# Kernel tuning notes

Measured on AMD Instinct MI355X. Metric: run time of the kernel, lower is better.

## Reference

```python
import jax, jax.numpy as jnp
import numpy as np

B, S, INP, HID = 64, 2048, 512, 512

def setup_inputs() -> dict:
    key = jax.random.key(0)
    ks = jax.random.split(key, 8)
    inp = jax.random.normal(ks[0], (B, INP), dtype=jnp.float32)
    context = jax.random.normal(ks[1], (B, S, INP), dtype=jnp.float32)
    mask = jax.random.randint(ks[2], (B, S), 0, 2) == 1  # True = masked out
    lim_l = 1.0 / np.sqrt(INP)
    Wl = jax.random.uniform(ks[3], (HID, INP), minval=-lim_l, maxval=lim_l, dtype=jnp.float32)
    bl = jax.random.uniform(ks[4], (HID,), minval=-lim_l, maxval=lim_l, dtype=jnp.float32)
    Wc = jax.random.uniform(ks[5], (HID, INP), minval=-lim_l, maxval=lim_l, dtype=jnp.float32)  # Conv1d k=1 weight squeezed
    bc = jax.random.uniform(ks[6], (HID,), minval=-lim_l, maxval=lim_l, dtype=jnp.float32)
    V = jax.random.uniform(ks[7], (HID,), minval=-1.0, maxval=1.0, dtype=jnp.float32)
    return {"inp": inp, "context": context, "mask": mask,
            "Wl": Wl, "bl": bl, "Wc": Wc, "bc": bc, "V": V}

def reference(inp, context, mask, Wl, bl, Wc, bc, V):
    # hid: [B, HID], broadcast over S
    hid = inp @ Wl.T + bl
    # 1x1 Conv1d over permuted context == per-position linear: [B, HID, S]
    ctx = jnp.einsum('bsi,hi->bhs', context, Wc) + bc[None, :, None]
    # additive attention scores: [B, S]
    att = jnp.einsum('h,bhs->bs', V, jnp.tanh(hid[:, :, None] + ctx))
    att = jnp.where(mask, -jnp.inf, att)
    alpha = jax.nn.softmax(att, axis=1)
    # context vector: [B, HID]
    hidden_state = jnp.einsum('bhs,bs->bh', ctx, alpha)
    return (hidden_state, alpha)
```

## Files before the change

kernel.cpp:

```cpp
#include <hip/hip_runtime.h>
#include <hip/hip_bf16.h>
#include <cstdint>
#include <cstddef>

#define B_   64
#define S_   2048
#define INP_ 512
#define HID_ 512
#define NCH_ 32

typedef float          floatx4  __attribute__((ext_vector_type(4)));
typedef __bf16         bf16x8   __attribute__((ext_vector_type(8)));
typedef unsigned short ushortx8 __attribute__((ext_vector_type(8)));
typedef unsigned short ushortx4 __attribute__((ext_vector_type(4)));

#define K2E 1.4426950408889634f

__device__ __forceinline__ unsigned short f2bf(float f) {
  unsigned u = __float_as_uint(f);
  u += 0x7FFFu + ((u >> 16) & 1u);
  return (unsigned short)(u >> 16);
}
__device__ __forceinline__ float bf2f(unsigned short h) {
  return __uint_as_float(((unsigned)h) << 16);
}
__device__ __forceinline__ float fast_tanh(float x) {
  float u = __builtin_amdgcn_exp2f(x * 2.88539008177792681472f);
  return 1.0f - 2.0f * __builtin_amdgcn_rcpf(u + 1.0f);
}

__device__ __forceinline__ int detect_mask_mode(const void* mask, int t, int* flags) {
  if (t == 0) *flags = 0;
  __syncthreads();
  int f = 0;
  const unsigned* mw = (const unsigned*)mask;
  for (int i = t; i < 512; i += 256) {
    unsigned v = mw[i];
    if (v > 1u) f |= 1;
    if (v != 0u && v != 0x3f800000u) f |= 2;
  }
  if (f) atomicOr(flags, f);
  __syncthreads();
  const int fl = *flags;
  return ((fl & 1) == 0) ? 0 : (((fl & 2) == 0) ? 1 : 2);
}
__device__ __forceinline__ bool mask_at(const void* mask, int mode, size_t idx) {
  if (mode == 0) return ((const int*)mask)[idx] != 0;
  if (mode == 1) return ((const float*)mask)[idx] != 0.0f;
  return ((const unsigned char*)mask)[idx] != 0;
}

__global__ __launch_bounds__(256) void prep_kernel(
    const float* __restrict__ inp, const float* __restrict__ Wl,
    const float* __restrict__ bl, float* __restrict__ hid,
    const float* __restrict__ Wc, unsigned short* __restrict__ pk)
{
  __shared__ float vs[512];
  const int t = threadIdx.x;
  if (blockIdx.x < 128) {
    int g = blockIdx.x * 256 + t;
    int l = g & 63, ks = (g >> 6) & 15, m16 = g >> 10;
    int row = m16 * 16 + (l & 15);
    int kb  = ks * 32 + (l >> 4) * 8;
    const float4* s = (const float4*)(Wc + (size_t)row * 512 + kb);
    float4 a = s[0], c = s[1];
    ushortx8 o = { f2bf(a.x), f2bf(a.y), f2bf(a.z), f2bf(a.w),
                   f2bf(c.x), f2bf(c.y), f2bf(c.z), f2bf(c.w) };
    *(ushortx8*)(pk + (size_t)g * 8) = o;
    return;
  }
  const int bx = blockIdx.x - 128;
  const int xo = bx & 7, b = bx >> 3;
  const int w = t >> 6, lane = t & 63;
  for (int i = t; i < 512; i += 256) vs[i] = inp[(size_t)b * 512 + i];
  __syncthreads();
  float vl[8];
  #pragma unroll
  for (int j = 0; j < 8; ++j) vl[j] = vs[lane * 8 + j];
  const int h0 = xo * 64 + w * 16;
  #pragma unroll
  for (int i = 0; i < 16; ++i) {
    const int h = h0 + i;
    const float4* wr = (const float4*)(Wl + (size_t)h * 512 + lane * 8);
    float4 w0 = wr[0], w1 = wr[1];
    float d = w0.x*vl[0] + w0.y*vl[1] + w0.z*vl[2] + w0.w*vl[3]
            + w1.x*vl[4] + w1.y*vl[5] + w1.z*vl[6] + w1.w*vl[7];
    #pragma unroll
    for (int off = 32; off; off >>= 1) d += __shfl_xor(d, off);
    if (lane == 0) hid[(size_t)b * 512 + h] = bl[h] + d;
  }
}

__global__ __launch_bounds__(256, 2) void att_gemm_kernel(
    const float* __restrict__ context, const unsigned short* __restrict__ Wc_pk,
    const float* __restrict__ hid, const float* __restrict__ bc,
    const float* __restrict__ V, const void* __restrict__ mask,
    float* __restrict__ att, float* __restrict__ partial,
    float* __restrict__ mt, float* __restrict__ lt)
{
  __shared__ alignas(16) unsigned short bsm[64 * 512];
  __shared__ float hid_sm[512];
  __shared__ float V_sm[512];
  __shared__ float bc_sm[512];
  __shared__ float att_sm[64];
  __shared__ float w_sm[64];
  __shared__ int   flags;

  const int b    = blockIdx.y;
  const int c    = blockIdx.x;
  const int s0   = c * 64;
  const int t    = threadIdx.x;
  const int lane = t & 63;
  const int w    = t >> 6;
  const int quad = lane >> 4;
  const int l15  = lane & 15;

  const int mode = detect_mask_mode(mask, t, &flags);

  for (int i = t; i < 512; i += 256) {
    hid_sm[i] = hid[b * 512 + i];
    V_sm[i]   = V[i];
    bc_sm[i]  = bc[i];
  }
  if (t < 64) att_sm[t] = 0.0f;

  floatx4 acc[8][4];
  #pragma unroll
  for (int m = 0; m < 8; ++m)
    #pragma unroll
    for (int n = 0; n < 4; ++n) { floatx4 z = {0.f,0.f,0.f,0.f}; acc[m][n] = z; }

  const unsigned short* apBase = Wc_pk + (size_t)(w * 8) * 8192 + lane * 8;
  const float* src = context + ((size_t)b * S_ + s0) * INP_;

  for (int phase = 0; phase < 4; ++phase) {
    __syncthreads();
    #pragma unroll
    for (int i = 0; i < 8; ++i) {
      int id  = t + i * 256;
      int row = id >> 5;
      int c4  = id & 31;
      float4 f = *(const float4*)(src + (size_t)row * INP_ + phase * 128 + c4 * 4);
      int chunk = c4 >> 1, half = c4 & 1;
      int sw = chunk ^ (row & 7);
      ushortx4 hv = { f2bf(f.x), f2bf(f.y), f2bf(f.z), f2bf(f.w) };
      *(ushortx4*)(&bsm[row * 512 + phase * 128 + sw * 8 + half * 4]) = hv;
    }
    __syncthreads();
    #pragma unroll
    for (int ksl = 0; ksl < 4; ++ksl) {
      const int ksg = phase * 4 + ksl;
      bf16x8 af[8];
      #pragma unroll
      for (int m = 0; m < 8; ++m)
        af[m] = *(const bf16x8*)(apBase + (size_t)m * 8192 + ksg * 512);
      bf16x8 bfr[4];
      #pragma unroll
      for (int n = 0; n < 4; ++n) {
        int row = n * 16 + l15;
        int cc  = ksl * 4 + quad;
        bfr[n] = *(const bf16x8*)(&bsm[row * 512 + phase * 128 + ((cc ^ (row & 7)) * 8)]);
      }
      #pragma unroll
      for (int m = 0; m < 8; ++m)
        #pragma unroll
        for (int n = 0; n < 4; ++n)
          acc[m][n] = __builtin_amdgcn_mfma_f32_16x16x32_bf16(af[m], bfr[n], acc[m][n], 0, 0, 0);
    }
  }

  float attacc[4] = {0.f, 0.f, 0.f, 0.f};
  #pragma unroll
  for (int m = 0; m < 8; ++m) {
    const int hb = w * 128 + m * 16 + quad * 4;
    #pragma unroll
    for (int r = 0; r < 4; ++r) {
      const int h = hb + r;
      const float base = hid_sm[h] + bc_sm[h];
      const float vv = V_sm[h];
      #pragma unroll
      for (int n = 0; n < 4; ++n)
        attacc[n] += vv * fast_tanh(base + acc[m][n][r]);
    }
  }
  #pragma unroll
  for (int n = 0; n < 4; ++n) {
    float v = attacc[n];
    v += __shfl_xor(v, 16);
    v += __shfl_xor(v, 32);
    if (lane < 16) atomicAdd(&att_sm[n * 16 + l15], v);
  }
  __syncthreads();

  if (t < 64) {
    att[(size_t)b * S_ + s0 + t] = att_sm[t];
    const bool m = mask_at(mask, mode, (size_t)b * S_ + s0 + t);
    const float av = att_sm[t];
    float mv = m ? -1e30f : av;
    #pragma unroll
    for (int off = 32; off; off >>= 1) mv = fmaxf(mv, __shfl_xor(mv, off));
    const float wv = m ? 0.0f : __builtin_amdgcn_exp2f((av - mv) * K2E);
    w_sm[t] = wv;
    float lv = wv;
    #pragma unroll
    for (int off = 32; off; off >>= 1) lv += __shfl_xor(lv, off);
    if (t == 0) { mt[b * NCH_ + c] = mv; lt[b * NCH_ + c] = lv; }
  }
  __syncthreads();

  {
    const int k0 = t * 2;
    const int p  = k0 >> 7, kl = k0 & 127;
    const int c4 = kl >> 2, j = kl & 3;
    const int idxu = p * 128 + (c4 >> 1) * 8 + (c4 & 1) * 4 + j;
    float ax = 0.f, ay = 0.f;
    #pragma unroll 8
    for (int s = 0; s < 64; ++s) {
      const unsigned v = *(const unsigned*)(&bsm[s * 512 + (idxu ^ ((s & 7) << 3))]);
      const float wv = w_sm[s];
      ax = fmaf(wv, bf2f((unsigned short)(v & 0xffffu)), ax);
      ay = fmaf(wv, bf2f((unsigned short)(v >> 16)), ay);
    }
    float2 o; o.x = ax; o.y = ay;
    *(float2*)(partial + ((size_t)c * B_ + b) * INP_ + k0) = o;
  }
}

__global__ __launch_bounds__(256) void finalize_kernel(
    const void* __restrict__ mask, const float* __restrict__ att,
    const float* __restrict__ mt, const float* __restrict__ lt,
    float* __restrict__ sc, float* __restrict__ alpha)
{
  __shared__ int flags;
  __shared__ float Msh, Lsh;
  const int b = blockIdx.x, t = threadIdx.x;
  const int mode = detect_mask_mode(mask, t, &flags);

  if (t < 32) {
    float m = mt[b * NCH_ + t];
    #pragma unroll
    for (int off = 16; off; off >>= 1) m = fmaxf(m, __shfl_xor(m, off));
    float e = __builtin_amdgcn_exp2f((mt[b * NCH_ + t] - m) * K2E) * lt[b * NCH_ + t];
    #pragma unroll
    for (int off = 16; off; off >>= 1) e += __shfl_xor(e, off);
    if (t == 0) { Msh = m; Lsh = e; }
  }
  __syncthreads();
  const float M = Msh;
  const float rL = 1.0f / Lsh;
  if (t < 32) sc[b * NCH_ + t] = __builtin_amdgcn_exp2f((mt[b * NCH_ + t] - M) * K2E) * rL;

  #pragma unroll
  for (int i = 0; i < 8; ++i) {
    const int idx = i * 256 + t;
    const bool m = mask_at(mask, mode, (size_t)b * S_ + idx);
    const float a = m ? 0.0f
                      : __builtin_amdgcn_exp2f((att[(size_t)b * S_ + idx] - M) * K2E) * rL;
    alpha[(size_t)b * S_ + idx] = a;
  }
}

__global__ __launch_bounds__(256) void hiddendot_kernel(
    const float* __restrict__ Wc, const float* __restrict__ bc,
    const float* __restrict__ partial, const float* __restrict__ sc,
    float* __restrict__ hidden)
{
  __shared__ float vs[512];
  __shared__ float scs[NCH_];
  const int b = blockIdx.y, t = threadIdx.x;
  const int w = t >> 6, lane = t & 63;
  if (t < NCH_) scs[t] = sc[b * NCH_ + t];
  __syncthreads();
  for (int i = t; i < 512; i += 256) {
    float s = 0.0f;
    #pragma unroll 4
    for (int c = 0; c < NCH_; ++c)
      s += scs[c] * partial[((size_t)c * B_ + b) * INP_ + i];
    vs[i] = s;
  }
  __syncthreads();
  float vl[8];
  #pragma unroll
  for (int j = 0; j < 8; ++j) vl[j] = vs[lane * 8 + j];
  const int h0 = blockIdx.x * 64 + w * 16;
  #pragma unroll
  for (int i = 0; i < 16; ++i) {
    const int h = h0 + i;
    const float4* wr = (const float4*)(Wc + (size_t)h * 512 + lane * 8);
    float4 w0 = wr[0], w1 = wr[1];
    float d = w0.x*vl[0] + w0.y*vl[1] + w0.z*vl[2] + w0.w*vl[3]
            + w1.x*vl[4] + w1.y*vl[5] + w1.z*vl[6] + w1.w*vl[7];
    #pragma unroll
    for (int off = 32; off; off >>= 1) d += __shfl_xor(d, off);
    if (lane == 0) hidden[(size_t)b * 512 + h] = bc[h] + d;
  }
}

extern "C" void kernel_launch(void* const* d_in, const int* in_sizes, int n_in,
                              void* d_out, int out_size, void* d_ws, size_t ws_size,
                              hipStream_t stream)
{
  const float* inp     = (const float*)d_in[0];
  const float* context = (const float*)d_in[1];
  const void*  mask    = d_in[2];
  const float* Wl      = (const float*)d_in[3];
  const float* bl      = (const float*)d_in[4];
  const float* Wc      = (const float*)d_in[5];
  const float* bc      = (const float*)d_in[6];
  const float* V       = (const float*)d_in[7];

  float* hidden = (float*)d_out;
  float* alpha  = (float*)d_out + B_ * HID_;

  char* ws = (char*)d_ws;
  const size_t HIDW = (size_t)B_ * HID_ * 4;
  const size_t ATT  = (size_t)B_ * S_ * 4;
  const size_t PK   = (size_t)HID_ * INP_ * 2;
  const size_t PART = (size_t)NCH_ * B_ * INP_ * 4;
  const size_t MT   = (size_t)B_ * NCH_ * 4;

  float* hid_ws      = (float*)ws;
  float* att_ws      = (float*)(ws + HIDW);
  unsigned short* pk = (unsigned short*)(ws + HIDW + ATT);
  float* partial     = (float*)(ws + HIDW + ATT + PK);
  float* mt          = (float*)(ws + HIDW + ATT + PK + PART);
  float* lt          = (float*)(ws + HIDW + ATT + PK + PART + MT);
  float* sc          = (float*)(ws + HIDW + ATT + PK + PART + 2 * MT);

  prep_kernel<<<640, 256, 0, stream>>>(inp, Wl, bl, hid_ws, Wc, pk);
  att_gemm_kernel<<<dim3(NCH_, B_), 256, 0, stream>>>(
      context, pk, hid_ws, bc, V, mask, att_ws, partial, mt, lt);
  finalize_kernel<<<B_, 256, 0, stream>>>(mask, att_ws, mt, lt, sc, alpha);
  hiddendot_kernel<<<dim3(HID_ / 64, B_), 256, 0, stream>>>(Wc, bc, partial, sc, hidden);
}
```

Measured before the change: 490.8 us.

## Halve sequence tile to 32 and software-pipeline context staging into shared memory

Shrinks each attention block's sequence tile from 64 to 32 positions, which doubles the chunk count, cuts LDS and accumulator use, and raises the occupancy hint to 3 blocks per SM. The context tile is now fully kept in LDS, with the next K-phase's global loads issued before the current phase's MFMAs and written after them, so load latency overlaps compute. The A fragments are loaded one at a time inside the m loop. In exchange, each block reuses every Wc fragment across half as many positions, so Wc traffic per output doubles, and the partial buffer and finalize work grow with the chunk count.

After: 560.3 us. 1.14x slower.

```diff
diff --git a/kernel.cpp b/kernel.cpp
--- a/kernel.cpp
+++ b/kernel.cpp
@@ -7,7 +7,8 @@
 #define S_   2048
 #define INP_ 512
 #define HID_ 512
-#define NCH_ 32
+#define STILE 32
+#define NCH_ 64
 
 typedef float          floatx4  __attribute__((ext_vector_type(4)));
 typedef __bf16         bf16x8   __attribute__((ext_vector_type(8)));
@@ -91,24 +92,24 @@
   }
 }
 
-__global__ __launch_bounds__(256, 2) void att_gemm_kernel(
+__global__ __launch_bounds__(256, 3) void att_gemm_kernel(
     const float* __restrict__ context, const unsigned short* __restrict__ Wc_pk,
     const float* __restrict__ hid, const float* __restrict__ bc,
     const float* __restrict__ V, const void* __restrict__ mask,
     float* __restrict__ att, float* __restrict__ partial,
     float* __restrict__ mt, float* __restrict__ lt)
 {
-  __shared__ alignas(16) unsigned short bsm[64 * 512];
+  __shared__ alignas(16) unsigned short bsm[STILE * 512];
   __shared__ float hid_sm[512];
   __shared__ float V_sm[512];
   __shared__ float bc_sm[512];
-  __shared__ float att_sm[64];
-  __shared__ float w_sm[64];
+  __shared__ float att_sm[STILE];
+  __shared__ float w_sm[STILE];
   __shared__ int   flags;
 
   const int b    = blockIdx.y;
   const int c    = blockIdx.x;
-  const int s0   = c * 64;
+  const int s0   = c * STILE;
   const int t    = threadIdx.x;
   const int lane = t & 63;
   const int w    = t >> 6;
@@ -122,54 +123,73 @@
     V_sm[i]   = V[i];
     bc_sm[i]  = bc[i];
   }
-  if (t < 64) att_sm[t] = 0.0f;
-
-  floatx4 acc[8][4];
+  if (t < STILE) att_sm[t] = 0.0f;
+
+  floatx4 acc[8][2];
   #pragma unroll
   for (int m = 0; m < 8; ++m)
     #pragma unroll
-    for (int n = 0; n < 4; ++n) { floatx4 z = {0.f,0.f,0.f,0.f}; acc[m][n] = z; }
+    for (int n = 0; n < 2; ++n) { floatx4 z = {0.f,0.f,0.f,0.f}; acc[m][n] = z; }
 
   const unsigned short* apBase = Wc_pk + (size_t)(w * 8) * 8192 + lane * 8;
   const float* src = context + ((size_t)b * S_ + s0) * INP_;
 
+  const int srow = t >> 5;
+  const int c4   = t & 31;
+  const int half = c4 & 1;
+  const int sw   = (c4 >> 1) ^ (srow & 7);
+  const int dst_off = sw * 8 + half * 4;
+
+  {
+    float4 stg[4];
+    #pragma unroll
+    for (int i = 0; i < 4; ++i)
+      stg[i] = *(const float4*)(src + (size_t)(srow + i * 8) * INP_ + c4 * 4);
+    #pragma unroll
+    for (int i = 0; i < 4; ++i) {
+      ushortx4 hv = { f2bf(stg[i].x), f2bf(stg[i].y), f2bf(stg[i].z), f2bf(stg[i].w) };
+      *(ushortx4*)(&bsm[(srow + i * 8) * 512 + dst_off]) = hv;
+    }
+  }
+  __syncthreads();
+
+  #pragma unroll
   for (int phase = 0; phase < 4; ++phase) {
-    __syncthreads();
-    #pragma unroll
-    for (int i = 0; i < 8; ++i) {
-      int id  = t + i * 256;
-      int row = id >> 5;
-      int c4  = id & 31;
-      float4 f = *(const float4*)(src + (size_t)row * INP_ + phase * 128 + c4 * 4);
-      int chunk = c4 >> 1, half = c4 & 1;
-      int sw = chunk ^ (row & 7);
-      ushortx4 hv = { f2bf(f.x), f2bf(f.y), f2bf(f.z), f2bf(f.w) };
-      *(ushortx4*)(&bsm[row * 512 + phase * 128 + sw * 8 + half * 4]) = hv;
-    }
-    __syncthreads();
+    float4 nst[4];
+    if (phase < 3) {
+      #pragma unroll
+      for (int i = 0; i < 4; ++i)
+        nst[i] = *(const float4*)(src + (size_t)(srow + i * 8) * INP_
+                                      + (phase + 1) * 128 + c4 * 4);
+    }
     #pragma unroll
     for (int ksl = 0; ksl < 4; ++ksl) {
       const int ksg = phase * 4 + ksl;
-      bf16x8 af[8];
-      #pragma unroll
-      for (int m = 0; m < 8; ++m)
-        af[m] = *(const bf16x8*)(apBase + (size_t)m * 8192 + ksg * 512);
-      bf16x8 bfr[4];
-      #pragma unroll
-      for (int n = 0; n < 4; ++n) {
+      bf16x8 bfr[2];
+      #pragma unroll
+      for (int n = 0; n < 2; ++n) {
         int row = n * 16 + l15;
         int cc  = ksl * 4 + quad;
         bfr[n] = *(const bf16x8*)(&bsm[row * 512 + phase * 128 + ((cc ^ (row & 7)) * 8)]);
       }
       #pragma unroll
-      for (int m = 0; m < 8; ++m)
-        #pragma unroll
-        for (int n = 0; n < 4; ++n)
-          acc[m][n] = __builtin_amdgcn_mfma_f32_16x16x32_bf16(af[m], bfr[n], acc[m][n], 0, 0, 0);
-    }
-  }
-
-  float attacc[4] = {0.f, 0.f, 0.f, 0.f};
+      for (int m = 0; m < 8; ++m) {
+        bf16x8 af = *(const bf16x8*)(apBase + (size_t)m * 8192 + ksg * 512);
+        acc[m][0] = __builtin_amdgcn_mfma_f32_16x16x32_bf16(af, bfr[0], acc[m][0], 0, 0, 0);
+        acc[m][1] = __builtin_amdgcn_mfma_f32_16x16x32_bf16(af, bfr[1], acc[m][1], 0, 0, 0);
+      }
+    }
+    if (phase < 3) {
+      #pragma unroll
+      for (int i = 0; i < 4; ++i) {
+        ushortx4 hv = { f2bf(nst[i].x), f2bf(nst[i].y), f2bf(nst[i].z), f2bf(nst[i].w) };
+        *(ushortx4*)(&bsm[(srow + i * 8) * 512 + (phase + 1) * 128 + dst_off]) = hv;
+      }
+    }
+    __syncthreads();
+  }
+
+  float attacc[2] = {0.f, 0.f};
   #pragma unroll
   for (int m = 0; m < 8; ++m) {
     const int hb = w * 128 + m * 16 + quad * 4;
@@ -179,12 +199,12 @@
       const float base = hid_sm[h] + bc_sm[h];
       const float vv = V_sm[h];
       #pragma unroll
-      for (int n = 0; n < 4; ++n)
+      for (int n = 0; n < 2; ++n)
         attacc[n] += vv * fast_tanh(base + acc[m][n][r]);
     }
   }
   #pragma unroll
-  for (int n = 0; n < 4; ++n) {
+  for (int n = 0; n < 2; ++n) {
     float v = attacc[n];
     v += __shfl_xor(v, 16);
     v += __shfl_xor(v, 32);
@@ -192,31 +212,28 @@
   }
   __syncthreads();
 
-  if (t < 64) {
+  if (t < STILE) {
     att[(size_t)b * S_ + s0 + t] = att_sm[t];
     const bool m = mask_at(mask, mode, (size_t)b * S_ + s0 + t);
     const float av = att_sm[t];
     float mv = m ? -1e30f : av;
     #pragma unroll
-    for (int off = 32; off; off >>= 1) mv = fmaxf(mv, __shfl_xor(mv, off));
+    for (int off = 16; off; off >>= 1) mv = fmaxf(mv, __shfl_xor(mv, off));
     const float wv = m ? 0.0f : __builtin_amdgcn_exp2f((av - mv) * K2E);
     w_sm[t] = wv;
     float lv = wv;
     #pragma unroll
-    for (int off = 32; off; off >>= 1) lv += __shfl_xor(lv, off);
+    for (int off = 16; off; off >>= 1) lv += __shfl_xor(lv, off);
     if (t == 0) { mt[b * NCH_ + c] = mv; lt[b * NCH_ + c] = lv; }
   }
   __syncthreads();
 
   {
     const int k0 = t * 2;
-    const int p  = k0 >> 7, kl = k0 & 127;
-    const int c4 = kl >> 2, j = kl & 3;
-    const int idxu = p * 128 + (c4 >> 1) * 8 + (c4 & 1) * 4 + j;
     float ax = 0.f, ay = 0.f;
     #pragma unroll 8
-    for (int s = 0; s < 64; ++s) {
-      const unsigned v = *(const unsigned*)(&bsm[s * 512 + (idxu ^ ((s & 7) << 3))]);
+    for (int s = 0; s < STILE; ++s) {
+      const unsigned v = *(const unsigned*)(&bsm[s * 512 + (k0 ^ ((s & 7) << 3))]);
       const float wv = w_sm[s];
       ax = fmaf(wv, bf2f((unsigned short)(v & 0xffffu)), ax);
       ay = fmaf(wv, bf2f((unsigned short)(v >> 16)), ay);
@@ -236,19 +253,19 @@
   const int b = blockIdx.x, t = threadIdx.x;
   const int mode = detect_mask_mode(mask, t, &flags);
 
-  if (t < 32) {
+  if (t < NCH_) {
     float m = mt[b * NCH_ + t];
     #pragma unroll
-    for (int off = 16; off; off >>= 1) m = fmaxf(m, __shfl_xor(m, off));
+    for (int off = 32; off; off >>= 1) m = fmaxf(m, __shfl_xor(m, off));
     float e = __builtin_amdgcn_exp2f((mt[b * NCH_ + t] - m) * K2E) * lt[b * NCH_ + t];
     #pragma unroll
-    for (int off = 16; off; off >>= 1) e += __shfl_xor(e, off);
+    for (int off = 32; off; off >>= 1) e += __shfl_xor(e, off);
     if (t == 0) { Msh = m; Lsh = e; }
   }
   __syncthreads();
   const float M = Msh;
   const float rL = 1.0f / Lsh;
-  if (t < 32) sc[b * NCH_ + t] = __builtin_amdgcn_exp2f((mt[b * NCH_ + t] - M) * K2E) * rL;
+  if (t < NCH_) sc[b * NCH_ + t] = __builtin_amdgcn_exp2f((mt[b * NCH_ + t] - M) * K2E) * rL;
 
   #pragma unroll
   for (int i = 0; i < 8; ++i) {
```

## Prefetch next context phase into LDS, hoist mask-mode detection, raise MFMA priority

Applied to the files above, without the earlier changes.

The GEMM loop now stages the next 128-column phase of the context tile into its own region of LDS before running MFMAs on the current phase, which removes one barrier per phase and lets global loads overlap compute. The mask-type detection moves out of every GEMM and finalize block into one extra prep block that writes the mode to workspace. s_setprio is raised around the MFMA bursts. Because the staging conversion and LDS writes sit in the same wave ahead of the MFMAs, the overlap depends on how the compiler schedules the code, and register pressure may rise.

New measurement: 479.1 us. -2.4%, faster.

```diff
diff --git a/kernel.cpp b/kernel.cpp
--- a/kernel.cpp
+++ b/kernel.cpp
@@ -7,6 +7,7 @@
 #define S_   2048
 #define INP_ 512
 #define HID_ 512
+#define STILE 64
 #define NCH_ 32
 
 typedef float          floatx4  __attribute__((ext_vector_type(4)));
@@ -29,21 +30,6 @@
   return 1.0f - 2.0f * __builtin_amdgcn_rcpf(u + 1.0f);
 }
 
-__device__ __forceinline__ int detect_mask_mode(const void* mask, int t, int* flags) {
-  if (t == 0) *flags = 0;
-  __syncthreads();
-  int f = 0;
-  const unsigned* mw = (const unsigned*)mask;
-  for (int i = t; i < 512; i += 256) {
-    unsigned v = mw[i];
-    if (v > 1u) f |= 1;
-    if (v != 0u && v != 0x3f800000u) f |= 2;
-  }
-  if (f) atomicOr(flags, f);
-  __syncthreads();
-  const int fl = *flags;
-  return ((fl & 1) == 0) ? 0 : (((fl & 2) == 0) ? 1 : 2);
-}
 __device__ __forceinline__ bool mask_at(const void* mask, int mode, size_t idx) {
   if (mode == 0) return ((const int*)mask)[idx] != 0;
   if (mode == 1) return ((const float*)mask)[idx] != 0.0f;
@@ -53,10 +39,30 @@
 __global__ __launch_bounds__(256) void prep_kernel(
     const float* __restrict__ inp, const float* __restrict__ Wl,
     const float* __restrict__ bl, float* __restrict__ hid,
-    const float* __restrict__ Wc, unsigned short* __restrict__ pk)
+    const float* __restrict__ Wc, unsigned short* __restrict__ pk,
+    const void* __restrict__ mask, int* __restrict__ mode_ws)
 {
   __shared__ float vs[512];
+  __shared__ int flags;
   const int t = threadIdx.x;
+  if (blockIdx.x == 640) {
+    if (t == 0) flags = 0;
+    __syncthreads();
+    int f = 0;
+    const unsigned* mw = (const unsigned*)mask;
+    for (int i = t; i < 512; i += 256) {
+      unsigned v = mw[i];
+      if (v > 1u) f |= 1;
+      if (v != 0u && v != 0x3f800000u) f |= 2;
+    }
+    if (f) atomicOr(&flags, f);
+    __syncthreads();
+    if (t == 0) {
+      const int fl = flags;
+      *mode_ws = ((fl & 1) == 0) ? 0 : (((fl & 2) == 0) ? 1 : 2);
+    }
+    return;
+  }
   if (blockIdx.x < 128) {
     int g = blockIdx.x * 256 + t;
     int l = g & 63, ks = (g >> 6) & 15, m16 = g >> 10;
@@ -95,34 +101,34 @@
     const float* __restrict__ context, const unsigned short* __restrict__ Wc_pk,
     const float* __restrict__ hid, const float* __restrict__ bc,
     const float* __restrict__ V, const void* __restrict__ mask,
+    const int* __restrict__ mode_ws,
     float* __restrict__ att, float* __restrict__ partial,
     float* __restrict__ mt, float* __restrict__ lt)
 {
-  __shared__ alignas(16) unsigned short bsm[64 * 512];
+  __shared__ alignas(16) unsigned short bsm[STILE * 512];
   __shared__ float hid_sm[512];
   __shared__ float V_sm[512];
   __shared__ float bc_sm[512];
-  __shared__ float att_sm[64];
-  __shared__ float w_sm[64];
-  __shared__ int   flags;
+  __shared__ float att_sm[STILE];
+  __shared__ float w_sm[STILE];
 
   const int b    = blockIdx.y;
   const int c    = blockIdx.x;
-  const int s0   = c * 64;
+  const int s0   = c * STILE;
   const int t    = threadIdx.x;
   const int lane = t & 63;
   const int w    = t >> 6;
   const int quad = lane >> 4;
   const int l15  = lane & 15;
 
-  const int mode = detect_mask_mode(mask, t, &flags);
+  const int mode = *mode_ws;
 
   for (int i = t; i < 512; i += 256) {
     hid_sm[i] = hid[b * 512 + i];
     V_sm[i]   = V[i];
     bc_sm[i]  = bc[i];
   }
-  if (t < 64) att_sm[t] = 0.0f;
+  if (t < STILE) att_sm[t] = 0.0f;
 
   floatx4 acc[8][4];
   #pragma unroll
@@ -133,20 +139,25 @@
   const unsigned short* apBase = Wc_pk + (size_t)(w * 8) * 8192 + lane * 8;
   const float* src = context + ((size_t)b * S_ + s0) * INP_;
 
-  for (int phase = 0; phase < 4; ++phase) {
-    __syncthreads();
+  auto stage = [&](int p) {
     #pragma unroll
     for (int i = 0; i < 8; ++i) {
       int id  = t + i * 256;
       int row = id >> 5;
       int c4  = id & 31;
-      float4 f = *(const float4*)(src + (size_t)row * INP_ + phase * 128 + c4 * 4);
+      float4 f = *(const float4*)(src + (size_t)row * INP_ + p * 128 + c4 * 4);
       int chunk = c4 >> 1, half = c4 & 1;
       int sw = chunk ^ (row & 7);
       ushortx4 hv = { f2bf(f.x), f2bf(f.y), f2bf(f.z), f2bf(f.w) };
-      *(ushortx4*)(&bsm[row * 512 + phase * 128 + sw * 8 + half * 4]) = hv;
-    }
-    __syncthreads();
+      *(ushortx4*)(&bsm[row * 512 + p * 128 + sw * 8 + half * 4]) = hv;
+    }
+  };
+
+  stage(0);
+  __syncthreads();
+
+  for (int phase = 0; phase < 4; ++phase) {
+    if (phase < 3) stage(phase + 1);
     #pragma unroll
     for (int ksl = 0; ksl < 4; ++ksl) {
       const int ksg = phase * 4 + ksl;
@@ -161,12 +172,15 @@
         int cc  = ksl * 4 + quad;
         bfr[n] = *(const bf16x8*)(&bsm[row * 512 + phase * 128 + ((cc ^ (row & 7)) * 8)]);
       }
+      __builtin_amdgcn_s_setprio(1);
       #pragma unroll
       for (int m = 0; m < 8; ++m)
         #pragma unroll
         for (int n = 0; n < 4; ++n)
           acc[m][n] = __builtin_amdgcn_mfma_f32_16x16x32_bf16(af[m], bfr[n], acc[m][n], 0, 0, 0);
-    }
+      __builtin_amdgcn_s_setprio(0);
+    }
+    __syncthreads();
   }
 
   float attacc[4] = {0.f, 0.f, 0.f, 0.f};
@@ -192,7 +206,7 @@
   }
   __syncthreads();
 
-  if (t < 64) {
+  if (t < STILE) {
     att[(size_t)b * S_ + s0 + t] = att_sm[t];
     const bool m = mask_at(mask, mode, (size_t)b * S_ + s0 + t);
     const float av = att_sm[t];
@@ -215,7 +229,7 @@
     const int idxu = p * 128 + (c4 >> 1) * 8 + (c4 & 1) * 4 + j;
     float ax = 0.f, ay = 0.f;
     #pragma unroll 8
-    for (int s = 0; s < 64; ++s) {
+    for (int s = 0; s < STILE; ++s) {
       const unsigned v = *(const unsigned*)(&bsm[s * 512 + (idxu ^ ((s & 7) << 3))]);
       const float wv = w_sm[s];
       ax = fmaf(wv, bf2f((unsigned short)(v & 0xffffu)), ax);
@@ -228,15 +242,15 @@
 
 __global__ __launch_bounds__(256) void finalize_kernel(
     const void* __restrict__ mask, const float* __restrict__ att,
+    const int* __restrict__ mode_ws,
     const float* __restrict__ mt, const float* __restrict__ lt,
     float* __restrict__ sc, float* __restrict__ alpha)
 {
-  __shared__ int flags;
   __shared__ float Msh, Lsh;
   const int b = blockIdx.x, t = threadIdx.x;
-  const int mode = detect_mask_mode(mask, t, &flags);
-
-  if (t < 32) {
+  const int mode = *mode_ws;
+
+  if (t < NCH_) {
     float m = mt[b * NCH_ + t];
     #pragma unroll
     for (int off = 16; off; off >>= 1) m = fmaxf(m, __shfl_xor(m, off));
@@ -248,7 +262,7 @@
   __syncthreads();
   const float M = Msh;
   const float rL = 1.0f / Lsh;
-  if (t < 32) sc[b * NCH_ + t] = __builtin_amdgcn_exp2f((mt[b * NCH_ + t] - M) * K2E) * rL;
+  if (t < NCH_) sc[b * NCH_ + t] = __builtin_amdgcn_exp2f((mt[b * NCH_ + t] - M) * K2E) * rL;
 
   #pragma unroll
   for (int i = 0; i < 8; ++i) {
@@ -326,10 +340,11 @@
   float* mt          = (float*)(ws + HIDW + ATT + PK + PART);
   float* lt          = (float*)(ws + HIDW + ATT + PK + PART + MT);
   float* sc          = (float*)(ws + HIDW + ATT + PK + PART + 2 * MT);
-
-  prep_kernel<<<640, 256, 0, stream>>>(inp, Wl, bl, hid_ws, Wc, pk);
+  int*   mode_ws     = (int*)  (ws + HIDW + ATT + PK + PART + 3 * MT);
+
+  prep_kernel<<<641, 256, 0, stream>>>(inp, Wl, bl, hid_ws, Wc, pk, mask, mode_ws);
   att_gemm_kernel<<<dim3(NCH_, B_), 256, 0, stream>>>(
-      context, pk, hid_ws, bc, V, mask, att_ws, partial, mt, lt);
-  finalize_kernel<<<B_, 256, 0, stream>>>(mask, att_ws, mt, lt, sc, alpha);
+      context, pk, hid_ws, bc, V, mask, mode_ws, att_ws, partial, mt, lt);
+  finalize_kernel<<<B_, 256, 0, stream>>>(mask, att_ws, mode_ws, mt, lt, sc, alpha);
   hiddendot_kernel<<<dim3(HID_ / 64, B_), 256, 0, stream>>>(Wc, bc, partial, sc, hidden);
 }
```
